# Kernel tuning notes

Hardware: AMD Instinct MI355X
Metric: run time of the kernel (lower is better)

The kernel has to match this reference:

```python
import jax, jax.numpy as jnp
from jax import lax
import numpy as np


def setup_inputs() -> dict:
    key = jax.random.key(0)
    kx, kw = jax.random.split(key)
    # Binary {0,1} activations: the module's int8-cast/XOR/AND trick is only
    # meaningful XNOR-popcount math for binary inputs.
    x = jax.random.randint(kx, (32, 256, 58, 58), 0, 2).astype(jnp.float32)
    weight = jax.random.normal(kw, (256, 256, 3, 3), dtype=jnp.float32)
    return {"x": x, "weight": weight}


def reference(x, weight):
    # XNORConv2d.forward, stride=1, padding=0 (forward never pads).
    B, C, H, W = x.shape
    O, _, kh, kw = weight.shape
    n = C * H * W  # note: alpha normalizes by INPUT size, as in the source
    N = kh * kw

    # alpha = sum_{c,kh,kw} |w| / n, one scalar per output filter  -> (O,)
    alpha = jnp.sum(jnp.abs(weight), axis=(1, 2, 3)) / n

    # Binarized weights: sign(w) >= 0 -> {0,1}
    bw = (weight >= 0).astype(x.dtype)

    dn = lax.conv_dimension_numbers(x.shape, weight.shape, ("NCHW", "OIHW", "NCHW"))
    conv = lambda a, f: lax.conv_general_dilated(
        a, f, window_strides=(1, 1), padding="VALID", dimension_numbers=dn
    )

    # XNOR match count per (b, o, y, x): S = #(p==f) over c,kh,kw
    #   = conv(p, f) + conv(1-p, 1-f)
    S = conv(x, bw) + conv(1.0 - x, 1.0 - bw)  # (B, O, H', W')

    # popcount per channel = 2*s_c - N; summed over channels -> 2*S - C*N
    res = 2.0 * S - jnp.asarray(C * N, dtype=x.dtype)

    return alpha[None, :, None, None] * res
```

## Files before the change

kernel.cpp:

```cpp
#include <hip/hip_runtime.h>
#include <stdint.h>


#define BATCH 32
#define C_IN 256
#define OCH 256
#define HIN 58
#define WIN2 58
#define HOUT 56
#define WOUT 56
#define TAPS 9
#define WWORDS 8
#define HWIN (HIN * WIN2)
#define HWOUT (HOUT * WOUT)
#define NPOS (BATCH * HWIN)

#define AP 144
#define NAPOS 232

typedef int   i32x4  __attribute__((ext_vector_type(4)));
typedef int   i32x16 __attribute__((ext_vector_type(16)));
typedef float f32x4  __attribute__((ext_vector_type(4)));

#define MFMA(acc, va, vb) \
    asm volatile("v_mfma_i32_32x32x32_i8 %0, %1, %2, %0" : "+a"(acc) : "v"(va), "v"(vb))

__global__ __launch_bounds__(256) void pack_x_kernel(
    const float* __restrict__ x, uint32_t* __restrict__ xp)
{
    int p = blockIdx.x * 256 + threadIdx.x;
    if (p >= NPOS) return;
    int b = p / HWIN;
    int r = p - b * HWIN;
    const float* xb = x + (size_t)b * C_IN * HWIN + r;
    uint32_t w[8];
    #pragma unroll
    for (int k = 0; k < 8; ++k) {
        uint32_t m = 0u;
        #pragma unroll
        for (int j = 0; j < 32; ++j)
            m |= (xb[(size_t)(k * 32 + j) * HWIN] > 0.5f ? 1u : 0u) << j;
        w[k] = m;
    }
    *(uint4*)(xp + (size_t)p * WWORDS)     = make_uint4(w[0], w[1], w[2], w[3]);
    *(uint4*)(xp + (size_t)p * WWORDS + 4) = make_uint4(w[4], w[5], w[6], w[7]);
}

__global__ __launch_bounds__(256) void pack_w8_kernel(
    const float* __restrict__ wt, char* __restrict__ wq8s, float* __restrict__ sA)
{
    int o = blockIdx.x;
    int c = threadIdx.x;
    const float* wb = wt + ((size_t)o * C_IN + c) * TAPS;
    float s = 0.f;
    char sg[TAPS];
    #pragma unroll
    for (int t = 0; t < TAPS; ++t) {
        float v = wb[t];
        s += fabsf(v);
        sg[t] = (v >= 0.0f) ? (char)1 : (char)-1;
    }
    int kh = c >> 7;
    int kb = (c >> 5) & 3;
    int e  = (c >> 4) & 1;
    int j  = c & 15;
    #pragma unroll
    for (int t = 0; t < TAPS; ++t) {
        int st = kh * 36 + t * 4 + kb;
        wq8s[(size_t)((st * 2 + e) * 256 + o) * 16 + j] = sg[t];
    }

    __shared__ float red[256];
    red[c] = s;
    __syncthreads();
    for (int off = 128; off > 0; off >>= 1) {
        if (c < off) red[c] += red[c + off];
        __syncthreads();
    }
    if (c == 0) sA[o] = red[0] / (float)(C_IN * HWIN);
}

__global__ __launch_bounds__(512)
__attribute__((amdgpu_waves_per_eu(4)))
void xnor_mfma_kernel(
    const uint32_t* __restrict__ xp, const char* __restrict__ wq8s,
    const float* __restrict__ sA, float* __restrict__ out)
{
    __shared__ __attribute__((aligned(16))) char lds[36864];
    char* Alds = lds;
    float* Cbuf = (float*)lds;

    int blk = blockIdx.x;
    int b   = blk / 28;
    int rp  = blk - b * 28;
    int oy0 = rp * 2;
    int tid  = threadIdx.x;
    int wv   = tid >> 6;
    int lane = tid & 63;
    int l31  = lane & 31;
    int e    = lane >> 5;
    int mgrp = wv & 1;
    int ngrp = wv >> 1;

    int baseA[2];
    #pragma unroll
    for (int mi = 0; mi < 2; ++mi) {
        int p = (mgrp * 2 + mi) * 32 + l31;
        int r = (p * 586) >> 15;
        int c = p - 56 * r;
        baseA[mi] = (r * 58 + c) * AP + e * 16;
    }
    const char* pb = wq8s + ((size_t)e * 256 + (size_t)(ngrp * 64 + l31)) * 16;
    float al0 = sA[ngrp * 64 + l31];
    float al1 = sA[ngrp * 64 + 32 + l31];

    i32x16 acc00 = {0}, acc01 = {0}, acc10 = {0}, acc11 = {0};
    asm volatile("" : "+a"(acc00), "+a"(acc01), "+a"(acc10), "+a"(acc11));
    asm volatile("s_nop 7\n\ts_nop 7");

#define KA(s) ((((((s) % 36) >> 2) / 3) * 58 + ((((s) % 36) >> 2) % 3)) * AP + ((s) & 3) * 32)

#define STAGE_A(KH)                                                        \
    {                                                                      \
        _Pragma("unroll")                                                  \
        for (int ir = 0; ir < 4; ++ir) {                                   \
            if (tid < 464) {                                               \
                int iw = tid >> 3, c16 = tid & 7;                          \
                uint32_t wvx = xp[((size_t)(b * HIN + oy0 + ir) * WIN2 + iw) * WWORDS \
                                  + (KH) * 4 + (c16 >> 1)];                \
                uint32_t bits = (c16 & 1) ? (wvx >> 16) : (wvx & 0xFFFFu); \
                i32x4 v;                                                   \
                _Pragma("unroll")                                          \
                for (int d = 0; d < 4; ++d) {                              \
                    uint32_t n  = (bits >> (4 * d)) & 0xFu;                \
                    uint32_t sp = (n * 0x204081u) & 0x01010101u;           \
                    v[d] = (int)~(sp * 0xFEu);                             \
                }                                                          \
                *(i32x4*)(Alds + (ir * 58 + iw) * AP + c16 * 16) = v;      \
            }                                                              \
        }                                                                  \
    }

    STAGE_A(0);

    i32x4 rb0[3], rb1[3];
    #pragma unroll
    for (int q = 0; q < 3; ++q) {
        rb0[q] = *(const i32x4*)(pb + (size_t)q * 8192);
        rb1[q] = *(const i32x4*)(pb + (size_t)q * 8192 + 512);
    }
    __syncthreads();

    i32x4 a0c = *(const i32x4*)(Alds + baseA[0] + KA(0));
    i32x4 a1c = *(const i32x4*)(Alds + baseA[1] + KA(0));

    #pragma unroll
    for (int s = 0; s < 72; ++s) {
        if (s == 36) {
            __syncthreads();
            STAGE_A(1);
            __syncthreads();
            a0c = *(const i32x4*)(Alds + baseA[0] + KA(36));
            a1c = *(const i32x4*)(Alds + baseA[1] + KA(36));
        }
        const int s3 = (s + 3 > 71) ? 71 : s + 3;
        i32x4 nb0 = *(const i32x4*)(pb + (size_t)s3 * 8192);
        i32x4 nb1 = *(const i32x4*)(pb + (size_t)s3 * 8192 + 512);
        const int sn = (s == 35 || s == 71) ? s : s + 1;
        i32x4 na0 = *(const i32x4*)(Alds + baseA[0] + KA(sn));
        i32x4 na1 = *(const i32x4*)(Alds + baseA[1] + KA(sn));

        i32x4 b0 = rb0[s % 3];
        i32x4 b1 = rb1[s % 3];
        MFMA(acc00, a0c, b0);
        MFMA(acc01, a0c, b1);
        MFMA(acc10, a1c, b0);
        MFMA(acc11, a1c, b1);

        rb0[s % 3] = nb0; rb1[s % 3] = nb1;
        a0c = na0; a1c = na1;
    }

    asm volatile("s_nop 7\n\ts_nop 7");

    size_t ob = ((size_t)b * OCH) * HWOUT + (size_t)oy0 * WOUT;
    #pragma unroll
    for (int q = 0; q < 4; ++q) {
        __syncthreads();
        if (mgrp == (q >> 1)) {
            const int mi = q & 1;
            #pragma unroll
            for (int ni = 0; ni < 2; ++ni) {
                float al = ni ? al1 : al0;
                int o = ngrp * 64 + ni * 32 + l31;
                i32x16 A;
                if (mi == 0 && ni == 0) A = acc00;
                else if (mi == 0)       A = acc01;
                else if (ni == 0)       A = acc10;
                else                    A = acc11;
                #pragma unroll
                for (int g = 0; g < 4; ++g) {
                    f32x4 vv;
                    vv[0] = al * (float)A[4 * g + 0];
                    vv[1] = al * (float)A[4 * g + 1];
                    vv[2] = al * (float)A[4 * g + 2];
                    vv[3] = al * (float)A[4 * g + 3];
                    int pl = g * 8 + 4 * e;
                    *(f32x4*)(Cbuf + (size_t)o * 36 + pl) = vv;
                }
            }
        }
        __syncthreads();
        #pragma unroll 1
        for (int i = 0; i < 16; ++i) {
            int idx = i * 512 + tid;
            int o = idx >> 5, pl = idx & 31;
            int pg = q * 32 + pl;
            if (pg < 112) {
                int r = (pg >= 56) ? 1 : 0;
                int c = pg - 56 * r;
                out[ob + (size_t)o * HWOUT + r * WOUT + c] = Cbuf[o * 36 + pl];
            }
        }
    }
#undef STAGE_A
#undef KA
}

extern "C" void kernel_launch(void* const* d_in, const int* in_sizes, int n_in,
                              void* d_out, int out_size, void* d_ws, size_t ws_size,
                              hipStream_t stream)
{
    const float* x  = (const float*)d_in[0];
    const float* wt = (const float*)d_in[1];
    float* out = (float*)d_out;

    char* ws = (char*)d_ws;
    uint32_t* xp   = (uint32_t*)ws;
    char*     wq8s = (char*)(ws + 3444736);
    float*    sAp  = (float*)(ws + 3444736 + 589824);

    pack_x_kernel<<<dim3((NPOS + 255) / 256), dim3(256), 0, stream>>>(x, xp);

    pack_w8_kernel<<<dim3(OCH), dim3(256), 0, stream>>>(wt, wq8s, sAp);

    xnor_mfma_kernel<<<dim3(896), dim3(512), 0, stream>>>(xp, wq8s, sAp, out);
}
```

Measured before the change: 301.9 us.

## Halve waves per block and give each wave a 64x128 MFMA tile

The MFMA kernel goes from 512 to 256 threads per block. Each wave now covers 128 output channels instead of 64, using 8 accumulators, so every A fragment read from LDS feeds four MFMAs instead of two. Weight prefetch depth drops from 3 to 2 stages to make room for the extra B registers. It also drops asm volatile on the MFMA so the compiler can schedule it, and removes the waves_per_eu hint. The gain is more reuse of A per LDS load, paid for with much higher accumulator register pressure and fewer waves to hide latency.

After: 473.7 us. 56.9% more time.

```diff
diff --git a/kernel.cpp b/kernel.cpp
--- a/kernel.cpp
+++ b/kernel.cpp
@@ -16,14 +16,13 @@
 #define NPOS (BATCH * HWIN)
 
 #define AP 144
-#define NAPOS 232
 
 typedef int   i32x4  __attribute__((ext_vector_type(4)));
 typedef int   i32x16 __attribute__((ext_vector_type(16)));
 typedef float f32x4  __attribute__((ext_vector_type(4)));
 
 #define MFMA(acc, va, vb) \
-    asm volatile("v_mfma_i32_32x32x32_i8 %0, %1, %2, %0" : "+a"(acc) : "v"(va), "v"(vb))
+    asm("v_mfma_i32_32x32x32_i8 %0, %1, %2, %0" : "+a"(acc) : "v"(va), "v"(vb))
 
 __global__ __launch_bounds__(256) void pack_x_kernel(
     const float* __restrict__ x, uint32_t* __restrict__ xp)
@@ -80,8 +79,7 @@
     if (c == 0) sA[o] = red[0] / (float)(C_IN * HWIN);
 }
 
-__global__ __launch_bounds__(512)
-__attribute__((amdgpu_waves_per_eu(4)))
+__global__ __launch_bounds__(256)
 void xnor_mfma_kernel(
     const uint32_t* __restrict__ xp, const char* __restrict__ wq8s,
     const float* __restrict__ sA, float* __restrict__ out)
@@ -110,12 +108,13 @@
         int c = p - 56 * r;
         baseA[mi] = (r * 58 + c) * AP + e * 16;
     }
-    const char* pb = wq8s + ((size_t)e * 256 + (size_t)(ngrp * 64 + l31)) * 16;
-    float al0 = sA[ngrp * 64 + l31];
-    float al1 = sA[ngrp * 64 + 32 + l31];
-
-    i32x16 acc00 = {0}, acc01 = {0}, acc10 = {0}, acc11 = {0};
-    asm volatile("" : "+a"(acc00), "+a"(acc01), "+a"(acc10), "+a"(acc11));
+    const char* pb = wq8s + ((size_t)e * 256 + (size_t)(ngrp * 128 + l31)) * 16;
+    float al[4];
+    #pragma unroll
+    for (int ni = 0; ni < 4; ++ni) al[ni] = sA[ngrp * 128 + ni * 32 + l31];
+
+    i32x16 acc00 = {0}, acc01 = {0}, acc02 = {0}, acc03 = {0};
+    i32x16 acc10 = {0}, acc11 = {0}, acc12 = {0}, acc13 = {0};
     asm volatile("s_nop 7\n\ts_nop 7");
 
 #define KA(s) ((((((s) % 36) >> 2) / 3) * 58 + ((((s) % 36) >> 2) % 3)) * AP + ((s) & 3) * 32)
@@ -123,9 +122,12 @@
 #define STAGE_A(KH)                                                        \
     {                                                                      \
         _Pragma("unroll")                                                  \
-        for (int ir = 0; ir < 4; ++ir) {                                   \
-            if (tid < 464) {                                               \
-                int iw = tid >> 3, c16 = tid & 7;                          \
+        for (int it = 0; it < 8; ++it) {                                   \
+            int L = it * 256 + tid;                                        \
+            if (L < 1856) {                                                \
+                int ir = L / 464;                                          \
+                int rem = L - ir * 464;                                    \
+                int iw = rem >> 3, c16 = rem & 7;                          \
                 uint32_t wvx = xp[((size_t)(b * HIN + oy0 + ir) * WIN2 + iw) * WWORDS \
                                   + (KH) * 4 + (c16 >> 1)];                \
                 uint32_t bits = (c16 & 1) ? (wvx >> 16) : (wvx & 0xFFFFu); \
@@ -143,11 +145,13 @@
 
     STAGE_A(0);
 
-    i32x4 rb0[3], rb1[3];
-    #pragma unroll
-    for (int q = 0; q < 3; ++q) {
+    i32x4 rb0[2], rb1[2], rb2[2], rb3[2];
+    #pragma unroll
+    for (int q = 0; q < 2; ++q) {
         rb0[q] = *(const i32x4*)(pb + (size_t)q * 8192);
         rb1[q] = *(const i32x4*)(pb + (size_t)q * 8192 + 512);
+        rb2[q] = *(const i32x4*)(pb + (size_t)q * 8192 + 1024);
+        rb3[q] = *(const i32x4*)(pb + (size_t)q * 8192 + 1536);
     }
     __syncthreads();
 
@@ -163,21 +167,29 @@
             a0c = *(const i32x4*)(Alds + baseA[0] + KA(36));
             a1c = *(const i32x4*)(Alds + baseA[1] + KA(36));
         }
-        const int s3 = (s + 3 > 71) ? 71 : s + 3;
-        i32x4 nb0 = *(const i32x4*)(pb + (size_t)s3 * 8192);
-        i32x4 nb1 = *(const i32x4*)(pb + (size_t)s3 * 8192 + 512);
+        const int s2 = (s + 2 > 71) ? 71 : s + 2;
+        i32x4 nb0 = *(const i32x4*)(pb + (size_t)s2 * 8192);
+        i32x4 nb1 = *(const i32x4*)(pb + (size_t)s2 * 8192 + 512);
+        i32x4 nb2 = *(const i32x4*)(pb + (size_t)s2 * 8192 + 1024);
+        i32x4 nb3 = *(const i32x4*)(pb + (size_t)s2 * 8192 + 1536);
         const int sn = (s == 35 || s == 71) ? s : s + 1;
         i32x4 na0 = *(const i32x4*)(Alds + baseA[0] + KA(sn));
         i32x4 na1 = *(const i32x4*)(Alds + baseA[1] + KA(sn));
 
-        i32x4 b0 = rb0[s % 3];
-        i32x4 b1 = rb1[s % 3];
+        i32x4 b0 = rb0[s & 1];
+        i32x4 b1 = rb1[s & 1];
+        i32x4 b2 = rb2[s & 1];
+        i32x4 b3 = rb3[s & 1];
         MFMA(acc00, a0c, b0);
         MFMA(acc01, a0c, b1);
+        MFMA(acc02, a0c, b2);
+        MFMA(acc03, a0c, b3);
         MFMA(acc10, a1c, b0);
         MFMA(acc11, a1c, b1);
-
-        rb0[s % 3] = nb0; rb1[s % 3] = nb1;
+        MFMA(acc12, a1c, b2);
+        MFMA(acc13, a1c, b3);
+
+        rb0[s & 1] = nb0; rb1[s & 1] = nb1; rb2[s & 1] = nb2; rb3[s & 1] = nb3;
         a0c = na0; a1c = na1;
     }
 
@@ -190,21 +202,28 @@
         if (mgrp == (q >> 1)) {
             const int mi = q & 1;
             #pragma unroll
-            for (int ni = 0; ni < 2; ++ni) {
-                float al = ni ? al1 : al0;
-                int o = ngrp * 64 + ni * 32 + l31;
+            for (int ni = 0; ni < 4; ++ni) {
+                int o = ngrp * 128 + ni * 32 + l31;
                 i32x16 A;
-                if (mi == 0 && ni == 0) A = acc00;
-                else if (mi == 0)       A = acc01;
-                else if (ni == 0)       A = acc10;
-                else                    A = acc11;
+                if (mi == 0) {
+                    if      (ni == 0) A = acc00;
+                    else if (ni == 1) A = acc01;
+                    else if (ni == 2) A = acc02;
+                    else              A = acc03;
+                } else {
+                    if      (ni == 0) A = acc10;
+                    else if (ni == 1) A = acc11;
+                    else if (ni == 2) A = acc12;
+                    else              A = acc13;
+                }
+                float alv = al[ni];
                 #pragma unroll
                 for (int g = 0; g < 4; ++g) {
                     f32x4 vv;
-                    vv[0] = al * (float)A[4 * g + 0];
-                    vv[1] = al * (float)A[4 * g + 1];
-                    vv[2] = al * (float)A[4 * g + 2];
-                    vv[3] = al * (float)A[4 * g + 3];
+                    vv[0] = alv * (float)A[4 * g + 0];
+                    vv[1] = alv * (float)A[4 * g + 1];
+                    vv[2] = alv * (float)A[4 * g + 2];
+                    vv[3] = alv * (float)A[4 * g + 3];
                     int pl = g * 8 + 4 * e;
                     *(f32x4*)(Cbuf + (size_t)o * 36 + pl) = vv;
                 }
@@ -212,8 +231,8 @@
         }
         __syncthreads();
         #pragma unroll 1
-        for (int i = 0; i < 16; ++i) {
-            int idx = i * 512 + tid;
+        for (int i = 0; i < 32; ++i) {
+            int idx = i * 256 + tid;
             int o = idx >> 5, pl = idx & 31;
             int pg = q * 32 + pl;
             if (pg < 112) {
@@ -244,5 +263,5 @@
 
     pack_w8_kernel<<<dim3(OCH), dim3(256), 0, stream>>>(wt, wq8s, sAp);
 
-    xnor_mfma_kernel<<<dim3(896), dim3(512), 0, stream>>>(xp, wq8s, sAp, out);
-}
+    xnor_mfma_kernel<<<dim3(896), dim3(256), 0, stream>>>(xp, wq8s, sAp, out);
+}
```
